# Optimization experiments

Hardware: AMD Instinct MI355X
Metric: run time of the kernel (lower is better)

The kernel has to match this reference:

```python
import jax, jax.numpy as jnp
import numpy as np

K = 10  # topk classes


def setup_inputs() -> dict:
    key = jax.random.key(0)
    ks = jax.random.split(key, 12)
    B, DF, M, C, V, DW, DT = 64, 768, 26, 3129, 10000, 300, 1024
    s = lambda k, sh, scale: jax.random.normal(k, sh, dtype=jnp.float32) * scale
    return {
        "ftm": s(ks[0], (B, DF, M, M), 1.0),
        "logits": s(ks[1], (B, C), 1.0),
        "labels": jax.random.randint(ks[2], (B,), 0, C, dtype=jnp.int32),
        "indices_table": jax.random.randint(ks[3], (C, 4), 0, V, dtype=jnp.int32),
        "word2vec": s(ks[4], (V, DW), 1.0),
        "W_emb": s(ks[5], (DW, DT), 1.0 / np.sqrt(DW)),
        "b_emb": jnp.zeros((DT,), jnp.float32),
        "W_cls": s(ks[6], (DT, DT), 1.0 / np.sqrt(DT)),
        "b_cls": jnp.zeros((DT,), jnp.float32),
        "W_v": s(ks[7], (DF, DT), 1.0 / np.sqrt(DF)),
        "b_v": jnp.zeros((DT,), jnp.float32),
        "W_bap": s(ks[8], (DT, DT), 1.0 / np.sqrt(DT)),
        "b_bap": jnp.zeros((DT,), jnp.float32),
        "W_fc": s(ks[9], (DT, K), 1.0 / np.sqrt(DT)),
        "b_fc": jnp.zeros((K,), jnp.float32),
    }


def reference(ftm, logits, labels, indices_table, word2vec,
              W_emb, b_emb, W_cls, b_cls, W_v, b_v, W_bap, b_bap, W_fc, b_fc):
    B, DF = ftm.shape[0], ftm.shape[1]
    C = logits.shape[1]
    # dispatch: topk classes, gather their word indices, embed
    _, topk_idx = jax.lax.top_k(logits, K)                  # [B, K]
    topk_cls = indices_table[topk_idx]                      # [B, K, 4]
    emb = word2vec[topk_cls].mean(axis=2)                   # [B, K, 300] (ClassEmbedding pooling)
    cls_emb = jax.nn.relu(emb @ W_emb + b_emb)              # [B, K, 1024]
    # SAC_BAP (dropouts in eval mode = identity)
    cls_emb = jax.nn.relu(cls_emb @ W_cls + b_cls)          # [B, K, 1024]
    f = ftm.reshape(B, DF, -1).transpose(0, 2, 1)           # [B, F, 768], F = m*m
    v = jax.nn.relu(f @ W_v + b_v)                          # [B, F, 1024]
    att_w_b_sfx = jnp.einsum('bfd,bkd->bfk', v, cls_emb)    # [B, F, K]
    att_w = jax.nn.softmax(att_w_b_sfx, axis=1)             # softmax over positions
    bap = jnp.einsum('bfd,bfk,bkd->bd', v, att_w, cls_emb)  # [B, 1024]
    bap = jax.nn.relu(bap @ W_bap + b_bap)                  # bap_emb_FC
    bap_logits = bap @ W_fc + b_fc                          # fc_new 1x1 conv -> [B, K]
    # combine: scatter topk logits into the full class space
    um = jnp.zeros((B, C), dtype=bap_logits.dtype)
    um = um.at[jnp.arange(B)[:, None], topk_idx].set(bap_logits)
    return um
```

## Files before the change

kernel.cpp:

```cpp
#include <hip/hip_runtime.h>
#include <hip/hip_bf16.h>

#define B_   64
#define C_   3129
#define K_   10
#define DF_  768
#define F_   676
#define DW_  300
#define DWP_ 320
#define DT_  1024
#define NSEG 13
#define FSEG 52

typedef __attribute__((ext_vector_type(8))) short short8;
typedef __attribute__((ext_vector_type(4))) float floatx4;

__device__ __forceinline__ void gload_lds16(const void* g, void* l) {
    __builtin_amdgcn_global_load_lds(
        (const __attribute__((address_space(1))) void*)g,
        (__attribute__((address_space(3))) void*)l, 16, 0, 0);
}

__global__ void topk_emb_kernel(const float* __restrict__ logits,
                                const int* __restrict__ indices_table,
                                const float* __restrict__ word2vec,
                                int* __restrict__ topk_idx,
                                __hip_bfloat16* __restrict__ emb) {
    __shared__ float vals[C_];
    __shared__ float red_v[256];
    __shared__ int   red_i[256];
    __shared__ int   sel[K_];
    int b = blockIdx.x;
    int tid = threadIdx.x;
    for (int i = tid; i < C_; i += 256) vals[i] = logits[(size_t)b * C_ + i];
    __syncthreads();
    for (int s = 0; s < K_; ++s) {
        float bv = -INFINITY; int bi = 0x7fffffff;
        for (int i = tid; i < C_; i += 256) {
            float v = vals[i];
            if (v > bv) { bv = v; bi = i; }
        }
        red_v[tid] = bv; red_i[tid] = bi;
        __syncthreads();
        for (int st = 128; st > 0; st >>= 1) {
            if (tid < st) {
                float ov = red_v[tid + st]; int oi = red_i[tid + st];
                if (ov > red_v[tid] || (ov == red_v[tid] && oi < red_i[tid])) {
                    red_v[tid] = ov; red_i[tid] = oi;
                }
            }
            __syncthreads();
        }
        if (tid == 0) {
            sel[s] = red_i[0];
            topk_idx[b * K_ + s] = red_i[0];
            vals[red_i[0]] = -INFINITY;
        }
        __syncthreads();
    }
    for (int idx = tid; idx < K_ * DWP_; idx += 256) {
        int j  = idx % DWP_;
        int kk = idx / DWP_;
        float s = 0.f;
        if (j < DW_) {
            const int* tbl = indices_table + (size_t)sel[kk] * 4;
            #pragma unroll
            for (int i = 0; i < 4; ++i) s += word2vec[(size_t)tbl[i] * DW_ + j];
            s *= 0.25f;
        }
        emb[((size_t)b * K_ + kk) * DWP_ + j] = (__hip_bfloat16)s;
    }
}

__device__ __forceinline__ void tp_body(const float* __restrict__ s,
                                        __hip_bfloat16* __restrict__ d,
                                        int R, int Cc, int Rp, int c0, int r0) {
    __shared__ float tile[64][65];
    int t = threadIdx.x;
    int cl = (t & 15) * 4;
    int rl = t >> 4;
    #pragma unroll
    for (int i = 0; i < 4; ++i) {
        int r = rl + i * 16;
        float4 v = make_float4(0.f, 0.f, 0.f, 0.f);
        if (r0 + r < R && c0 + cl < Cc)
            v = *(const float4*)(s + (size_t)(r0 + r) * Cc + c0 + cl);
        tile[r][cl + 0] = v.x; tile[r][cl + 1] = v.y;
        tile[r][cl + 2] = v.z; tile[r][cl + 3] = v.w;
    }
    __syncthreads();
    int cw = t >> 2;
    int r4 = (t & 3) * 16;
    if (c0 + cw < Cc) {
        __align__(16) __hip_bfloat16 buf[16];
        #pragma unroll
        for (int j = 0; j < 16; ++j) buf[j] = (__hip_bfloat16)tile[r4 + j][cw];
        float4* dp = (float4*)(d + (size_t)(c0 + cw) * Rp + r0 + r4);
        dp[0] = *(float4*)&buf[0];
        dp[1] = *(float4*)&buf[8];
    }
}

__global__ __launch_bounds__(256)
void transpose_ftm(const float* __restrict__ src, __hip_bfloat16* __restrict__ dst) {
    tp_body(src + (size_t)blockIdx.z * DF_ * F_,
            dst + (size_t)blockIdx.z * F_ * DF_,
            DF_, F_, DF_, blockIdx.x * 64, blockIdx.y * 64);
}

__global__ __launch_bounds__(256)
void transpose_weights(const float* __restrict__ Wemb, __hip_bfloat16* __restrict__ WembT,
                       const float* __restrict__ Wcls, __hip_bfloat16* __restrict__ WclsT,
                       const float* __restrict__ Wv,   __hip_bfloat16* __restrict__ WvT,
                       const float* __restrict__ Wbap, __hip_bfloat16* __restrict__ WbapT) {
    int id = blockIdx.x;
    const float* s; __hip_bfloat16* d; int R, Rp;
    if (id < 80)       { s = Wemb; d = WembT; R = DW_;  Rp = DWP_; }
    else if (id < 336) { s = Wcls; d = WclsT; R = DT_;  Rp = DT_;  id -= 80;  }
    else if (id < 528) { s = Wv;   d = WvT;   R = DF_;  Rp = DF_;  id -= 336; }
    else               { s = Wbap; d = WbapT; R = DT_;  Rp = DT_;  id -= 528; }
    int bx = id & 15;
    int by = id >> 4;
    tp_body(s, d, R, DT_, Rp, bx * 64, by * 64);
}

__global__ __launch_bounds__(256)
void transpose_all(const float* __restrict__ Wemb, __hip_bfloat16* __restrict__ WembT,
                   const float* __restrict__ Wcls, __hip_bfloat16* __restrict__ WclsT,
                   const float* __restrict__ Wv,   __hip_bfloat16* __restrict__ WvT,
                   const float* __restrict__ Wbap, __hip_bfloat16* __restrict__ WbapT,
                   const float* __restrict__ ftm,  __hip_bfloat16* __restrict__ ftm_t) {
    int id = blockIdx.x;
    if (id >= 784) {
        id -= 784;
        int z = id / 132;
        int t2 = id % 132;
        int bx = t2 % 11, by = t2 / 11;
        tp_body(ftm + (size_t)z * DF_ * F_, ftm_t + (size_t)z * F_ * DF_,
                DF_, F_, DF_, bx * 64, by * 64);
        return;
    }
    const float* s; __hip_bfloat16* d; int R, Rp;
    if (id < 80)       { s = Wemb; d = WembT; R = DW_;  Rp = DWP_; }
    else if (id < 336) { s = Wcls; d = WclsT; R = DT_;  Rp = DT_;  id -= 80;  }
    else if (id < 528) { s = Wv;   d = WvT;   R = DF_;  Rp = DF_;  id -= 336; }
    else               { s = Wbap; d = WbapT; R = DT_;  Rp = DT_;  id -= 528; }
    int bx = id & 15;
    int by = id >> 4;
    tp_body(s, d, R, DT_, Rp, bx * 64, by * 64);
}

template <int RELU, int OUTBF>
__global__ __launch_bounds__(256)
void gemm_mfma(const __hip_bfloat16* __restrict__ A,
               const __hip_bfloat16* __restrict__ Bt,
               const float* __restrict__ bias,
               void* __restrict__ Cout, int M, int N, int Kp) {
    __shared__ __align__(16) char smem[34816];
    __hip_bfloat16* As = (__hip_bfloat16*)smem;
    __hip_bfloat16* Bs = As + 128 * 64;
    int tid = threadIdx.x;
    int wave = tid >> 6, lane = tid & 63;
    int quad = lane >> 4, l16 = lane & 15;
    int wm = (wave & 1) * 64, wn = (wave >> 1) * 64;

    int gx = gridDim.x;
    int nwg = gx * gridDim.y;
    int flat = blockIdx.y * gx + blockIdx.x;
    int q = nwg >> 3, r = nwg & 7;
    int xcd = flat & 7, lid = flat >> 3;
    int o = (xcd < r ? xcd * (q + 1) : r * (q + 1) + (xcd - r) * q) + lid;
    int n0 = (o % gx) * 128;
    int m0 = (o / gx) * 128;

    floatx4 acc[4][4];
    #pragma unroll
    for (int i = 0; i < 4; ++i)
        #pragma unroll
        for (int j = 0; j < 4; ++j)
            acc[i][j] = (floatx4){0.f, 0.f, 0.f, 0.f};

    int rsub = lane >> 3;
    int gchunk = (lane & 7) ^ rsub;

    int arow[4], brow[4];
    #pragma unroll
    for (int i = 0; i < 4; ++i) {
        arow[i] = wm + i * 16 + l16;
        brow[i] = wn + i * 16 + l16;
    }

    for (int k0 = 0; k0 < Kp; k0 += 64) {
        #pragma unroll
        for (int c = 0; c < 4; ++c) {
            int grp = wave * 4 + c;
            int row = grp * 8 + rsub;
            int ra = m0 + row; if (ra >= M) ra = M - 1;
            gload_lds16(A + (size_t)ra * Kp + k0 + gchunk * 8, As + grp * 512);
            gload_lds16(Bt + (size_t)(n0 + row) * Kp + k0 + gchunk * 8, Bs + grp * 512);
        }
        __syncthreads();
        #pragma unroll
        for (int ks = 0; ks < 2; ++ks) {
            short8 af[4], bf[4];
            #pragma unroll
            for (int mi = 0; mi < 4; ++mi)
                af[mi] = *(const short8*)&As[arow[mi] * 64 +
                            ((((ks << 2) | quad) ^ (arow[mi] & 7)) << 3)];
            #pragma unroll
            for (int ni = 0; ni < 4; ++ni)
                bf[ni] = *(const short8*)&Bs[brow[ni] * 64 +
                            ((((ks << 2) | quad) ^ (brow[ni] & 7)) << 3)];
            #pragma unroll
            for (int mi = 0; mi < 4; ++mi)
                #pragma unroll
                for (int ni = 0; ni < 4; ++ni)
                    acc[mi][ni] = __builtin_amdgcn_mfma_f32_16x16x32_bf16(
                        af[mi], bf[ni], acc[mi][ni], 0, 0, 0);
        }
        __syncthreads();
    }

    float bn[4];
    #pragma unroll
    for (int ni = 0; ni < 4; ++ni) bn[ni] = bias[n0 + wn + ni * 16 + l16];

    if (OUTBF) {
        __hip_bfloat16* Cs = (__hip_bfloat16*)smem;
        #pragma unroll
        for (int mi = 0; mi < 4; ++mi)
            #pragma unroll
            for (int rr = 0; rr < 4; ++rr) {
                int row = wm + mi * 16 + quad * 4 + rr;
                #pragma unroll
                for (int ni = 0; ni < 4; ++ni) {
                    float val = acc[mi][ni][rr] + bn[ni];
                    if (RELU) val = fmaxf(val, 0.f);
                    Cs[row * 136 + wn + ni * 16 + l16] = (__hip_bfloat16)val;
                }
            }
        __syncthreads();
        #pragma unroll
        for (int j = 0; j < 8; ++j) {
            int ch = tid + 256 * j;
            int row = ch >> 4, c16 = ch & 15;
            int r = m0 + row;
            float4 val = *(const float4*)&Cs[row * 136 + c16 * 8];
            if (r < M)
                *(float4*)((__hip_bfloat16*)Cout + (size_t)r * N + n0 + c16 * 8) = val;
        }
    } else {
        #pragma unroll
        for (int mi = 0; mi < 4; ++mi)
            #pragma unroll
            for (int rr = 0; rr < 4; ++rr) {
                int r = m0 + wm + mi * 16 + quad * 4 + rr;
                if (r < M) {
                    #pragma unroll
                    for (int ni = 0; ni < 4; ++ni) {
                        float val = acc[mi][ni][rr] + bn[ni];
                        if (RELU) val = fmaxf(val, 0.f);
                        ((float*)Cout)[(size_t)r * N + n0 + wn + ni * 16 + l16] = val;
                    }
                }
            }
    }
}

__global__ __launch_bounds__(256)
void attn_s_mfma(const __hip_bfloat16* __restrict__ v_buf,
                 const __hip_bfloat16* __restrict__ cls,
                 float* __restrict__ s_buf, int b0) {
    __shared__ __align__(16) __hip_bfloat16 As[128 * 64];
    __shared__ __align__(16) __hip_bfloat16 Bs[16 * 64];
    int tid = threadIdx.x;
    int wave = tid >> 6, lane = tid & 63;
    int quad = lane >> 4, l16 = lane & 15;
    int bc = blockIdx.y;
    int b = b0 + bc;
    int f0 = blockIdx.x * 128;
    int wm = wave * 32;

    int rsub = lane >> 3;
    int gchunk = (lane & 7) ^ rsub;

    floatx4 acc[2];
    acc[0] = (floatx4){0.f, 0.f, 0.f, 0.f};
    acc[1] = (floatx4){0.f, 0.f, 0.f, 0.f};

    int arow[2];
    arow[0] = wm + l16;
    arow[1] = wm + 16 + l16;

    for (int k0 = 0; k0 < DT_; k0 += 64) {
        #pragma unroll
        for (int c = 0; c < 4; ++c) {
            int grp = wave * 4 + c;
            int row = grp * 8 + rsub;
            int fa = f0 + row; if (fa >= F_) fa = F_ - 1;
            gload_lds16(v_buf + ((size_t)bc * F_ + fa) * DT_ + k0 + gchunk * 8,
                        As + grp * 512);
        }
        if (wave == 0) {
            #pragma unroll
            for (int c = 0; c < 2; ++c) {
                int row = c * 8 + rsub;
                int rc = row < K_ ? row : K_ - 1;
                gload_lds16(cls + ((size_t)b * K_ + rc) * DT_ + k0 + gchunk * 8,
                            Bs + c * 512);
            }
        }
        __syncthreads();
        #pragma unroll
        for (int ks = 0; ks < 2; ++ks) {
            short8 bf = *(const short8*)&Bs[l16 * 64 +
                            ((((ks << 2) | quad) ^ (l16 & 7)) << 3)];
            #pragma unroll
            for (int mi = 0; mi < 2; ++mi) {
                short8 af = *(const short8*)&As[arow[mi] * 64 +
                                ((((ks << 2) | quad) ^ (arow[mi] & 7)) << 3)];
                acc[mi] = __builtin_amdgcn_mfma_f32_16x16x32_bf16(
                    af, bf, acc[mi], 0, 0, 0);
            }
        }
        __syncthreads();
    }

    if (l16 < K_) {
        #pragma unroll
        for (int mi = 0; mi < 2; ++mi)
            #pragma unroll
            for (int rr = 0; rr < 4; ++rr) {
                int f = f0 + wm + mi * 16 + quad * 4 + rr;
                if (f < F_)
                    s_buf[((size_t)bc * F_ + f) * K_ + l16] = acc[mi][rr];
            }
    }
}

__global__ __launch_bounds__(64)
void softmax_stats(const float* __restrict__ s_buf, float2* __restrict__ ml,
                   int b0) {
    int k = blockIdx.x, bc = blockIdx.y, lane = threadIdx.x;
    const float* sp = s_buf + (size_t)bc * F_ * K_ + k;
    float m = -INFINITY;
    for (int f = lane; f < F_; f += 64) m = fmaxf(m, sp[(size_t)f * K_]);
    #pragma unroll
    for (int off = 32; off > 0; off >>= 1) m = fmaxf(m, __shfl_xor(m, off));
    float l = 0.f;
    for (int f = lane; f < F_; f += 64) l += __expf(sp[(size_t)f * K_] - m);
    #pragma unroll
    for (int off = 32; off > 0; off >>= 1) l += __shfl_xor(l, off);
    if (lane == 0) ml[(size_t)(b0 + bc) * K_ + k] = make_float2(m, 1.f / l);
}

__global__ __launch_bounds__(256)
void o_bap_partial(const __hip_bfloat16* __restrict__ v_buf,
                   const float* __restrict__ s_buf,
                   const float2* __restrict__ ml,
                   const __hip_bfloat16* __restrict__ cls,
                   float* __restrict__ pp, int b0) {
    int bc = blockIdx.x, seg = blockIdx.y;
    int b = b0 + bc;
    int t = threadIdx.x;
    int f0 = seg * FSEG;
    __shared__ float wbuf[FSEG * K_];
    __shared__ float mk[K_], rlk[K_];
    __shared__ float red[128 * 8];
    if (t < K_) {
        float2 v = ml[(size_t)b * K_ + t];
        mk[t] = v.x; rlk[t] = v.y;
    }
    __syncthreads();
    for (int j = t; j < FSEG * K_; j += 256) {
        int k = j % K_;
        float sv = s_buf[((size_t)bc * F_ + f0) * K_ + j];
        wbuf[j] = __expf(sv - mk[k]) * rlk[k];
    }
    __syncthreads();
    int th = t & 127, half = t >> 7;
    int d0 = th * 8;
    int fs = half * (FSEG / 2);
    float acc[K_][8] = {};
    const __hip_bfloat16* vp = v_buf + ((size_t)bc * F_ + f0 + fs) * DT_ + d0;
    for (int f = 0; f < FSEG / 2; ++f) {
        union { float4 f4; __hip_bfloat16 h[8]; } u;
        u.f4 = *(const float4*)(vp + (size_t)f * DT_);
        float vv[8];
        #pragma unroll
        for (int i = 0; i < 8; ++i) vv[i] = (float)u.h[i];
        const float* wk = &wbuf[(fs + f) * K_];
        #pragma unroll
        for (int k = 0; k < K_; ++k)
            #pragma unroll
            for (int i = 0; i < 8; ++i) acc[k][i] += wk[k] * vv[i];
    }
    float outv[8] = {};
    union { float4 f4; __hip_bfloat16 h[8]; } cu;
    #pragma unroll
    for (int k = 0; k < K_; ++k) {
        cu.f4 = *(const float4*)(cls + ((size_t)b * K_ + k) * DT_ + d0);
        #pragma unroll
        for (int i = 0; i < 8; ++i) outv[i] += acc[k][i] * (float)cu.h[i];
    }
    if (half == 1) {
        *(float4*)&red[th * 8]     = *(float4*)&outv[0];
        *(float4*)&red[th * 8 + 4] = *(float4*)&outv[4];
    }
    __syncthreads();
    if (half == 0) {
        #pragma unroll
        for (int i = 0; i < 8; ++i) outv[i] += red[th * 8 + i];
        float* pd = pp + ((size_t)seg * B_ + b) * DT_ + d0;
        *(float4*)pd       = *(float4*)&outv[0];
        *(float4*)(pd + 4) = *(float4*)&outv[4];
    }
}

__global__ void bap_combine(const float* __restrict__ pp,
                            __hip_bfloat16* __restrict__ bap) {
    int idx = blockIdx.x * 256 + threadIdx.x;
    float s = 0.f;
    #pragma unroll
    for (int g = 0; g < NSEG; ++g) s += pp[idx + (size_t)g * B_ * DT_];
    bap[idx] = (__hip_bfloat16)s;
}

__global__ void final_kernel(const float* __restrict__ y,
                             const float* __restrict__ Wfc,
                             const float* __restrict__ bfc,
                             const int* __restrict__ topk_idx,
                             float* __restrict__ out) {
    int b = blockIdx.x, tid = threadIdx.x;
    int lane = tid & 63, wave = tid >> 6;
    float pk[K_] = {};
    for (int d = tid; d < DT_; d += 256) {
        float yv = y[(size_t)b * DT_ + d];
        #pragma unroll
        for (int k = 0; k < K_; ++k) pk[k] += yv * Wfc[(size_t)d * K_ + k];
    }
    __shared__ float wsum[4][K_];
    #pragma unroll
    for (int k = 0; k < K_; ++k) {
        float a = pk[k];
        #pragma unroll
        for (int off = 32; off > 0; off >>= 1) a += __shfl_down(a, off);
        if (lane == 0) wsum[wave][k] = a;
    }
    __syncthreads();
    if (tid < K_) {
        float lg = wsum[0][tid] + wsum[1][tid] + wsum[2][tid] + wsum[3][tid] + bfc[tid];
        out[(size_t)b * C_ + topk_idx[b * K_ + tid]] = lg;
    }
}

extern "C" void kernel_launch(void* const* d_in, const int* in_sizes, int n_in,
                              void* d_out, int out_size, void* d_ws, size_t ws_size,
                              hipStream_t stream) {
    const float* ftm           = (const float*)d_in[0];
    const float* logits        = (const float*)d_in[1];
    const int*   indices_table = (const int*)d_in[3];
    const float* word2vec      = (const float*)d_in[4];
    const float* W_emb         = (const float*)d_in[5];
    const float* b_emb         = (const float*)d_in[6];
    const float* W_cls         = (const float*)d_in[7];
    const float* b_cls         = (const float*)d_in[8];
    const float* W_v           = (const float*)d_in[9];
    const float* b_v           = (const float*)d_in[10];
    const float* W_bap         = (const float*)d_in[11];
    const float* b_bap         = (const float*)d_in[12];
    const float* W_fc          = (const float*)d_in[13];
    const float* b_fc          = (const float*)d_in[14];
    float* out = (float*)d_out;

    char* ws = (char*)d_ws;
    size_t off = 0;
    auto alloc = [&](size_t bytes) -> void* {
        void* p = ws + off;
        off = (off + bytes + 255) & ~(size_t)255;
        return p;
    };
    int*            topk_idx = (int*)           alloc((size_t)B_ * K_ * 4);
    __hip_bfloat16* emb_bf   = (__hip_bfloat16*)alloc((size_t)B_ * K_ * DWP_ * 2);
    __hip_bfloat16* cls1     = (__hip_bfloat16*)alloc((size_t)B_ * K_ * DT_ * 2);
    __hip_bfloat16* cls2     = (__hip_bfloat16*)alloc((size_t)B_ * K_ * DT_ * 2);
    __hip_bfloat16* Wemb_t   = (__hip_bfloat16*)alloc((size_t)DT_ * DWP_ * 2);
    __hip_bfloat16* Wcls_t   = (__hip_bfloat16*)alloc((size_t)DT_ * DT_ * 2);
    __hip_bfloat16* Wv_t     = (__hip_bfloat16*)alloc((size_t)DT_ * DF_ * 2);
    __hip_bfloat16* Wbap_t   = (__hip_bfloat16*)alloc((size_t)DT_ * DT_ * 2);
    float*          s_buf    = (float*)         alloc((size_t)B_ * F_ * K_ * 4);
    float2*         ml       = (float2*)        alloc((size_t)B_ * K_ * 8);
    float*          pp       = (float*)         alloc((size_t)NSEG * B_ * DT_ * 4);
    __hip_bfloat16* bap_bf   = (__hip_bfloat16*)alloc((size_t)B_ * DT_ * 2);
    float*          yb       = (float*)         alloc((size_t)B_ * DT_ * 4);

    size_t per_b = (size_t)F_ * DF_ * 2 + (size_t)F_ * DT_ * 2;
    size_t avail = (ws_size > off + 8192) ? ws_size - off - 8192 : 0;
    int nb = (int)(avail / per_b);
    if (nb > B_) nb = B_;
    if (nb < 1) nb = 1;
    __hip_bfloat16* ftm_t = (__hip_bfloat16*)alloc((size_t)nb * F_ * DF_ * 2);
    __hip_bfloat16* v_buf = (__hip_bfloat16*)alloc((size_t)nb * F_ * DT_ * 2);

    hipMemsetAsync(d_out, 0, (size_t)out_size * sizeof(float), stream);

    topk_emb_kernel<<<B_, 256, 0, stream>>>(logits, indices_table, word2vec,
                                            topk_idx, emb_bf);

    if (nb == B_) {
        transpose_all<<<784 + 132 * B_, 256, 0, stream>>>(
            W_emb, Wemb_t, W_cls, Wcls_t, W_v, Wv_t, W_bap, Wbap_t, ftm, ftm_t);
    } else {
        transpose_weights<<<784, 256, 0, stream>>>(
            W_emb, Wemb_t, W_cls, Wcls_t, W_v, Wv_t, W_bap, Wbap_t);
    }

    gemm_mfma<1, 1><<<dim3(DT_ / 128, (B_ * K_ + 127) / 128), 256, 0, stream>>>(
        emb_bf, Wemb_t, b_emb, cls1, B_ * K_, DT_, DWP_);
    gemm_mfma<1, 1><<<dim3(DT_ / 128, (B_ * K_ + 127) / 128), 256, 0, stream>>>(
        cls1, Wcls_t, b_cls, cls2, B_ * K_, DT_, DT_);

    for (int b0 = 0; b0 < B_; b0 += nb) {
        int cb = min(nb, B_ - b0);
        if (nb != B_) {
            transpose_ftm<<<dim3((F_ + 63) / 64, DF_ / 64, cb), 256, 0, stream>>>(
                ftm + (size_t)b0 * DF_ * F_, ftm_t);
        }
        int M = cb * F_;
        gemm_mfma<1, 1><<<dim3(DT_ / 128, (M + 127) / 128), 256, 0, stream>>>(
            ftm_t, Wv_t, b_v, v_buf, M, DT_, DF_);
        float* s_c = s_buf + (size_t)b0 * F_ * K_;
        attn_s_mfma<<<dim3((F_ + 127) / 128, cb), 256, 0, stream>>>(
            v_buf, cls2, s_c, b0);
        softmax_stats<<<dim3(K_, cb), 64, 0, stream>>>(s_c, ml, b0);
        o_bap_partial<<<dim3(cb, NSEG), 256, 0, stream>>>(
            v_buf, s_c, ml, cls2, pp, b0);
    }
    bap_combine<<<B_ * DT_ / 256, 256, 0, stream>>>(pp, bap_bf);

    gemm_mfma<1, 0><<<dim3(DT_ / 128, 1), 256, 0, stream>>>(
        bap_bf, Wbap_t, b_bap, yb, B_, DT_, DT_);
    final_kernel<<<B_, 256, 0, stream>>>(yb, W_fc, b_fc, topk_idx, out);
}
```

Baseline: 462.8 us.

## Fuse softmax stats into attention scores and fuse tail combine/GEMM/FC

The attention-score kernel now computes per-block partial softmax max/sum statistics with an online merge, which removes the separate softmax_stats kernel. o_bap_partial merges these per-block partials itself. The segment-sum combine, the bap GEMM, ReLU and the final 10-class FC are fused into one kernel that writes its results with atomicAdd. The aim is to cut kernel launches and intermediate buffer traffic. The cost is that each of the 8 tail blocks redundantly re-reads and sums all 13 pp segments, and half the waves compute unused rows.

```diff
diff --git a/kernel.cpp b/kernel.cpp
--- a/kernel.cpp
+++ b/kernel.cpp
@@ -11,6 +11,7 @@
 #define DT_  1024
 #define NSEG 13
 #define FSEG 52
+#define ASB  6
 
 typedef __attribute__((ext_vector_type(8))) short short8;
 typedef __attribute__((ext_vector_type(4))) float floatx4;
@@ -270,9 +271,11 @@
 __global__ __launch_bounds__(256)
 void attn_s_mfma(const __hip_bfloat16* __restrict__ v_buf,
                  const __hip_bfloat16* __restrict__ cls,
-                 float* __restrict__ s_buf, int b0) {
+                 float* __restrict__ s_buf, float2* __restrict__ pstats,
+                 int b0) {
     __shared__ __align__(16) __hip_bfloat16 As[128 * 64];
     __shared__ __align__(16) __hip_bfloat16 Bs[16 * 64];
+    __shared__ float2 wred[4][16];
     int tid = threadIdx.x;
     int wave = tid >> 6, lane = tid & 63;
     int quad = lane >> 4, l16 = lane & 15;
@@ -336,28 +339,53 @@
                     s_buf[((size_t)bc * F_ + f) * K_ + l16] = acc[mi][rr];
             }
     }
-}
-
-__global__ __launch_bounds__(64)
-void softmax_stats(const float* __restrict__ s_buf, float2* __restrict__ ml,
-                   int b0) {
-    int k = blockIdx.x, bc = blockIdx.y, lane = threadIdx.x;
-    const float* sp = s_buf + (size_t)bc * F_ * K_ + k;
-    float m = -INFINITY;
-    for (int f = lane; f < F_; f += 64) m = fmaxf(m, sp[(size_t)f * K_]);
-    #pragma unroll
-    for (int off = 32; off > 0; off >>= 1) m = fmaxf(m, __shfl_xor(m, off));
-    float l = 0.f;
-    for (int f = lane; f < F_; f += 64) l += __expf(sp[(size_t)f * K_] - m);
-    #pragma unroll
-    for (int off = 32; off > 0; off >>= 1) l += __shfl_xor(l, off);
-    if (lane == 0) ml[(size_t)(b0 + bc) * K_ + k] = make_float2(m, 1.f / l);
+
+    float mp = -INFINITY, lp = 0.f;
+    #pragma unroll
+    for (int mi = 0; mi < 2; ++mi)
+        #pragma unroll
+        for (int rr = 0; rr < 4; ++rr) {
+            int f = f0 + wm + mi * 16 + quad * 4 + rr;
+            if (f < F_) mp = fmaxf(mp, acc[mi][rr]);
+        }
+    if (mp > -INFINITY) {
+        #pragma unroll
+        for (int mi = 0; mi < 2; ++mi)
+            #pragma unroll
+            for (int rr = 0; rr < 4; ++rr) {
+                int f = f0 + wm + mi * 16 + quad * 4 + rr;
+                if (f < F_) lp += __expf(acc[mi][rr] - mp);
+            }
+    }
+    #pragma unroll
+    for (int off = 16; off < 64; off <<= 1) {
+        float mo = __shfl_xor(mp, off);
+        float lo = __shfl_xor(lp, off);
+        float mn = fmaxf(mp, mo);
+        float ln = (mp > -INFINITY ? lp * __expf(mp - mn) : 0.f)
+                 + (mo > -INFINITY ? lo * __expf(mo - mn) : 0.f);
+        mp = mn; lp = ln;
+    }
+    if (lane < 16) wred[wave][l16] = make_float2(mp, lp);
+    __syncthreads();
+    if (wave == 0 && lane < K_) {
+        float m = -INFINITY, l = 0.f;
+        #pragma unroll
+        for (int w = 0; w < 4; ++w) {
+            float2 p = wred[w][lane];
+            float mn = fmaxf(m, p.x);
+            l = (m > -INFINITY ? l * __expf(m - mn) : 0.f)
+              + (p.x > -INFINITY ? p.y * __expf(p.x - mn) : 0.f);
+            m = mn;
+        }
+        pstats[((size_t)bc * ASB + blockIdx.x) * K_ + lane] = make_float2(m, l);
+    }
 }
 
 __global__ __launch_bounds__(256)
 void o_bap_partial(const __hip_bfloat16* __restrict__ v_buf,
                    const float* __restrict__ s_buf,
-                   const float2* __restrict__ ml,
+                   const float2* __restrict__ pstats,
                    const __hip_bfloat16* __restrict__ cls,
                    float* __restrict__ pp, int b0) {
     int bc = blockIdx.x, seg = blockIdx.y;
@@ -368,8 +396,16 @@
     __shared__ float mk[K_], rlk[K_];
     __shared__ float red[128 * 8];
     if (t < K_) {
-        float2 v = ml[(size_t)b * K_ + t];
-        mk[t] = v.x; rlk[t] = v.y;
+        float m = -INFINITY, l = 0.f;
+        #pragma unroll
+        for (int j = 0; j < ASB; ++j) {
+            float2 p = pstats[((size_t)bc * ASB + j) * K_ + t];
+            float mn = fmaxf(m, p.x);
+            l = (m > -INFINITY ? l * __expf(m - mn) : 0.f)
+              + (p.x > -INFINITY ? p.y * __expf(p.x - mn) : 0.f);
+            m = mn;
+        }
+        mk[t] = m; rlk[t] = 1.f / l;
     }
     __syncthreads();
     for (int j = t; j < FSEG * K_; j += 256) {
@@ -417,40 +453,128 @@
     }
 }
 
-__global__ void bap_combine(const float* __restrict__ pp,
-                            __hip_bfloat16* __restrict__ bap) {
-    int idx = blockIdx.x * 256 + threadIdx.x;
-    float s = 0.f;
-    #pragma unroll
-    for (int g = 0; g < NSEG; ++g) s += pp[idx + (size_t)g * B_ * DT_];
-    bap[idx] = (__hip_bfloat16)s;
-}
-
-__global__ void final_kernel(const float* __restrict__ y,
-                             const float* __restrict__ Wfc,
-                             const float* __restrict__ bfc,
-                             const int* __restrict__ topk_idx,
-                             float* __restrict__ out) {
-    int b = blockIdx.x, tid = threadIdx.x;
-    int lane = tid & 63, wave = tid >> 6;
-    float pk[K_] = {};
-    for (int d = tid; d < DT_; d += 256) {
-        float yv = y[(size_t)b * DT_ + d];
-        #pragma unroll
-        for (int k = 0; k < K_; ++k) pk[k] += yv * Wfc[(size_t)d * K_ + k];
-    }
-    __shared__ float wsum[4][K_];
-    #pragma unroll
-    for (int k = 0; k < K_; ++k) {
-        float a = pk[k];
-        #pragma unroll
-        for (int off = 32; off > 0; off >>= 1) a += __shfl_down(a, off);
-        if (lane == 0) wsum[wave][k] = a;
-    }
-    __syncthreads();
-    if (tid < K_) {
-        float lg = wsum[0][tid] + wsum[1][tid] + wsum[2][tid] + wsum[3][tid] + bfc[tid];
-        out[(size_t)b * C_ + topk_idx[b * K_ + tid]] = lg;
+__global__ __launch_bounds__(256)
+void gemm_bap_final(const float* __restrict__ pp,
+                    const __hip_bfloat16* __restrict__ Bt,
+                    const float* __restrict__ b_bap,
+                    const float* __restrict__ Wfc,
+                    const float* __restrict__ bfc,
+                    const int* __restrict__ topk_idx,
+                    float* __restrict__ out) {
+    __shared__ __align__(16) __hip_bfloat16 As[128 * 64];
+    __shared__ __align__(16) __hip_bfloat16 Bs[128 * 64];
+    __shared__ float Wfc_s[128 * K_];
+    int tid = threadIdx.x;
+    int wave = tid >> 6, lane = tid & 63;
+    int quad = lane >> 4, l16 = lane & 15;
+    int wm = (wave & 1) * 64, wn = (wave >> 1) * 64;
+    int n0 = blockIdx.x * 128;
+
+    for (int i = tid; i < 128 * K_; i += 256)
+        Wfc_s[i] = Wfc[(size_t)(n0 + i / K_) * K_ + (i % K_)];
+
+    floatx4 acc[4][4];
+    #pragma unroll
+    for (int i = 0; i < 4; ++i)
+        #pragma unroll
+        for (int j = 0; j < 4; ++j)
+            acc[i][j] = (floatx4){0.f, 0.f, 0.f, 0.f};
+
+    int rsub = lane >> 3;
+    int gchunk = (lane & 7) ^ rsub;
+
+    int arow[4], brow[4];
+    #pragma unroll
+    for (int i = 0; i < 4; ++i) {
+        arow[i] = wm + i * 16 + l16;
+        brow[i] = wn + i * 16 + l16;
+    }
+
+    for (int k0 = 0; k0 < DT_; k0 += 64) {
+        #pragma unroll
+        for (int c = 0; c < 4; ++c) {
+            int grp = wave * 4 + c;
+            int row = grp * 8 + rsub;
+            gload_lds16(Bt + (size_t)(n0 + row) * DT_ + k0 + gchunk * 8,
+                        Bs + grp * 512);
+        }
+        #pragma unroll
+        for (int cc = 0; cc < 2; ++cc) {
+            int cell = tid + cc * 256;
+            int row = cell >> 3, chunk = cell & 7;
+            int slot = chunk ^ (row & 7);
+            const float* sp = pp + (size_t)row * DT_ + k0 + chunk * 8;
+            float4 aa = make_float4(0.f, 0.f, 0.f, 0.f);
+            float4 bb = make_float4(0.f, 0.f, 0.f, 0.f);
+            for (int sg = 0; sg < NSEG; ++sg) {
+                const float4* p4 = (const float4*)(sp + (size_t)sg * (B_ * DT_));
+                float4 x = p4[0], y = p4[1];
+                aa.x += x.x; aa.y += x.y; aa.z += x.z; aa.w += x.w;
+                bb.x += y.x; bb.y += y.y; bb.z += y.z; bb.w += y.w;
+            }
+            union { short8 s8; __hip_bfloat16 h[8]; } u;
+            u.h[0] = (__hip_bfloat16)aa.x; u.h[1] = (__hip_bfloat16)aa.y;
+            u.h[2] = (__hip_bfloat16)aa.z; u.h[3] = (__hip_bfloat16)aa.w;
+            u.h[4] = (__hip_bfloat16)bb.x; u.h[5] = (__hip_bfloat16)bb.y;
+            u.h[6] = (__hip_bfloat16)bb.z; u.h[7] = (__hip_bfloat16)bb.w;
+            *(short8*)&As[row * 64 + slot * 8] = u.s8;
+        }
+        __syncthreads();
+        #pragma unroll
+        for (int ks = 0; ks < 2; ++ks) {
+            short8 af[4], bf[4];
+            #pragma unroll
+            for (int mi = 0; mi < 4; ++mi)
+                af[mi] = *(const short8*)&As[arow[mi] * 64 +
+                            ((((ks << 2) | quad) ^ (arow[mi] & 7)) << 3)];
+            #pragma unroll
+            for (int ni = 0; ni < 4; ++ni)
+                bf[ni] = *(const short8*)&Bs[brow[ni] * 64 +
+                            ((((ks << 2) | quad) ^ (brow[ni] & 7)) << 3)];
+            #pragma unroll
+            for (int mi = 0; mi < 4; ++mi)
+                #pragma unroll
+                for (int ni = 0; ni < 4; ++ni)
+                    acc[mi][ni] = __builtin_amdgcn_mfma_f32_16x16x32_bf16(
+                        af[mi], bf[ni], acc[mi][ni], 0, 0, 0);
+        }
+        __syncthreads();
+    }
+
+    if (wm == 0) {
+        float bn[4];
+        #pragma unroll
+        for (int ni = 0; ni < 4; ++ni) bn[ni] = b_bap[n0 + wn + ni * 16 + l16];
+        #pragma unroll
+        for (int mi = 0; mi < 4; ++mi)
+            #pragma unroll
+            for (int rr = 0; rr < 4; ++rr) {
+                int r = mi * 16 + quad * 4 + rr;
+                float rowk[K_];
+                #pragma unroll
+                for (int k = 0; k < K_; ++k) rowk[k] = 0.f;
+                #pragma unroll
+                for (int ni = 0; ni < 4; ++ni) {
+                    int nl = wn + ni * 16 + l16;
+                    float val = fmaxf(acc[mi][ni][rr] + bn[ni], 0.f);
+                    const float* wf = &Wfc_s[nl * K_];
+                    #pragma unroll
+                    for (int k = 0; k < K_; ++k) rowk[k] += val * wf[k];
+                }
+                #pragma unroll
+                for (int off = 1; off < 16; off <<= 1)
+                    #pragma unroll
+                    for (int k = 0; k < K_; ++k)
+                        rowk[k] += __shfl_xor(rowk[k], off);
+                if (l16 == 0) {
+                    #pragma unroll
+                    for (int k = 0; k < K_; ++k) {
+                        float add = rowk[k];
+                        if (blockIdx.x == 0 && wave == 0) add += bfc[k];
+                        atomicAdd(&out[(size_t)r * C_ + topk_idx[r * K_ + k]], add);
+                    }
+                }
+            }
     }
 }
 
@@ -489,10 +613,8 @@
     __hip_bfloat16* Wv_t     = (__hip_bfloat16*)alloc((size_t)DT_ * DF_ * 2);
     __hip_bfloat16* Wbap_t   = (__hip_bfloat16*)alloc((size_t)DT_ * DT_ * 2);
     float*          s_buf    = (float*)         alloc((size_t)B_ * F_ * K_ * 4);
-    float2*         ml       = (float2*)        alloc((size_t)B_ * K_ * 8);
+    float2*         pstats   = (float2*)        alloc((size_t)B_ * ASB * K_ * 8);
     float*          pp       = (float*)         alloc((size_t)NSEG * B_ * DT_ * 4);
-    __hip_bfloat16* bap_bf   = (__hip_bfloat16*)alloc((size_t)B_ * DT_ * 2);
-    float*          yb       = (float*)         alloc((size_t)B_ * DT_ * 4);
 
     size_t per_b = (size_t)F_ * DF_ * 2 + (size_t)F_ * DT_ * 2;
     size_t avail = (ws_size > off + 8192) ? ws_size - off - 8192 : 0;
@@ -530,15 +652,12 @@
         gemm_mfma<1, 1><<<dim3(DT_ / 128, (M + 127) / 128), 256, 0, stream>>>(
             ftm_t, Wv_t, b_v, v_buf, M, DT_, DF_);
         float* s_c = s_buf + (size_t)b0 * F_ * K_;
-        attn_s_mfma<<<dim3((F_ + 127) / 128, cb), 256, 0, stream>>>(
-            v_buf, cls2, s_c, b0);
-        softmax_stats<<<dim3(K_, cb), 64, 0, stream>>>(s_c, ml, b0);
+        attn_s_mfma<<<dim3(ASB, cb), 256, 0, stream>>>(
+            v_buf, cls2, s_c, pstats, b0);
         o_bap_partial<<<dim3(cb, NSEG), 256, 0, stream>>>(
-            v_buf, s_c, ml, cls2, pp, b0);
-    }
-    bap_combine<<<B_ * DT_ / 256, 256, 0, stream>>>(pp, bap_bf);
-
-    gemm_mfma<1, 0><<<dim3(DT_ / 128, 1), 256, 0, stream>>>(
-        bap_bf, Wbap_t, b_bap, yb, B_, DT_, DT_);
-    final_kernel<<<B_, 256, 0, stream>>>(yb, W_fc, b_fc, topk_idx, out);
-}
+            v_buf, s_c, pstats, cls2, pp, b0);
+    }
+
+    gemm_bap_final<<<dim3(DT_ / 128, 1), 256, 0, stream>>>(
+        pp, Wbap_t, b_bap, W_fc, b_fc, topk_idx, out);
+}
```

Measured after the change: 573.6 us. 23.9% more time.
